# Kernel tuning notes

Hardware: AMD Instinct MI355X
Metric: run time of the kernel (lower is better)

Reference implementation:

```python
import jax, jax.numpy as jnp
import numpy as np

IN = 128      # input_size
HID = 64      # fast_net hidden width
NFW = IN * HID + HID  # 8256 flat fast weights (layer1 then layer2)
B = 256


def setup_inputs() -> dict:
    key = jax.random.key(0)
    k1, k2, k3, k4 = jax.random.split(key, 4)
    x = jax.random.normal(k1, (B, 1, IN), dtype=jnp.float32)
    # updater network weights: Linear(IN, 2*NFW, bias=False) then Linear(2*NFW, NFW, bias=False)
    W1 = jax.random.normal(k2, (2 * NFW, IN), dtype=jnp.float32) * 0.02
    W2 = jax.random.normal(k3, (NFW, 2 * NFW), dtype=jnp.float32) * 0.02
    # initial flat fast weights, in (0,1) since the update squashes there
    fw0 = jax.random.uniform(k4, (NFW,), dtype=jnp.float32)
    return {"x": x, "W1": W1, "W2": W2, "fw0": fw0}


def reference(x, W1, W2, fw0):
    xs = x[:, 0, :]  # [B, IN]
    # updater network has no weight updates itself -> batch the two matmuls
    U = (xs @ W1.T) @ W2.T  # [B, NFW] per-sample weight updates
    gain, shift = jnp.float32(10.0), jnp.float32(0.5)

    def step(fw, inp):
        x_i, u_i = inp
        # update_func: 1 / (1 + exp(-10*(w + u - 0.5)))
        fw = jax.nn.sigmoid(gain * (fw + u_i - shift))
        w1 = fw[: IN * HID].reshape(HID, IN)   # fast layer 1 [HID, IN]
        w2 = fw[IN * HID:].reshape(1, HID)     # fast layer 2 [1, HID]
        pred = w2 @ jax.nn.relu(w1 @ x_i)      # [1]
        return fw, pred

    _, preds = jax.lax.scan(step, fw0, (xs, U))  # sequential over batch, state persists
    return preds  # [B, 1]
```

## Files before the change

kernel.cpp:

```cpp
#include <hip/hip_runtime.h>
#include <hip/hip_bf16.h>

#define IN_DIM 128
#define HID    64
#define NFW    8256
#define BATCH  256
#define K2     16512
#define BM     96
#define NMB    86
#define KSPLIT 6
#define NT_PER 43
#define GRID_M 516

typedef float f32x4 __attribute__((ext_vector_type(4)));
typedef short bf16x8 __attribute__((ext_vector_type(8)));

__device__ __forceinline__ unsigned int f2bf(float f) {
    union { float f; unsigned int u; } v; v.f = f;
    return (v.u + 0x7FFFu + ((v.u >> 16) & 1u)) >> 16;
}

__global__ __launch_bounds__(256) void k_prep_w1t(const float* __restrict__ W1,
                                                  unsigned short* __restrict__ W1T) {
    __shared__ float tile[64][IN_DIM + 1];
    const int kt = blockIdx.x;
    const int t  = threadIdx.x;
    const float* src = W1 + (size_t)kt * 64 * IN_DIM;
#pragma unroll
    for (int p = 0; p < 8; ++p) {
        int c4 = p * 256 + t;
        int e = c4 * 4;
        int row = e >> 7, col = e & 127;
        f32x4 v = *reinterpret_cast<const f32x4*>(src + row * IN_DIM + col);
        tile[row][col+0] = v.x; tile[row][col+1] = v.y;
        tile[row][col+2] = v.z; tile[row][col+3] = v.w;
    }
    __syncthreads();
    unsigned short* dst = W1T + (size_t)kt * (IN_DIM * 64);
#pragma unroll
    for (int it = 0; it < 4; ++it) {
        int c = it * 256 + t;
        int n = c >> 3, kl0 = (c & 7) * 8;
        uint4 w;
        w.x = f2bf(tile[kl0+0][n]) | (f2bf(tile[kl0+1][n]) << 16);
        w.y = f2bf(tile[kl0+2][n]) | (f2bf(tile[kl0+3][n]) << 16);
        w.z = f2bf(tile[kl0+4][n]) | (f2bf(tile[kl0+5][n]) << 16);
        w.w = f2bf(tile[kl0+6][n]) | (f2bf(tile[kl0+7][n]) << 16);
        *reinterpret_cast<uint4*>(dst + c * 8) = w;
    }
}

__global__ __launch_bounds__(256, 2) void k_gemm_M(const float* __restrict__ W2,
                                                   const unsigned short* __restrict__ W1T,
                                                   float* __restrict__ Mpart) {
    __shared__ __align__(16) unsigned char smem[57344];
    float* trs = reinterpret_cast<float*>(smem);

    const int t = threadIdx.x;
    const int lane = t & 63, wid = t >> 6;
    const int wm = wid >> 1, wn = wid & 1;
    const int l15 = lane & 15, l4 = (lane >> 4) & 3;

    const int b = blockIdx.x;
    const int xcd = b & 7, slot = b >> 3;
    const int p = (xcd < 4) ? (xcd * 65 + slot) : (260 + (xcd - 4) * 64 + slot);
    const int ks = p / NMB, mb = p % NMB;

    const int m0 = mb * BM;
    const int g0 = ks * NT_PER;
    const int kt0 = (p * 7) % NT_PER;

    const int ar  = t >> 3;
    const int asw = (ar & 7) << 4;
    const float* abase = W2 + (size_t)(m0 + ar) * K2 + (size_t)g0 * 64 + (t & 7) * 8;
    const int bn  = t >> 1;
    const int bsw = (bn & 7) << 4;
    const unsigned short* bbase = W1T + (size_t)g0 * 8192 + bn * 64 + (t & 1) * 32;

    f32x4 sa0, sa1, sa2, sa3, sa4, sa5;
    uint4 sb0, sb1, sb2, sb3;
    f32x4 acc[3][4];
#pragma unroll
    for (int mf = 0; mf < 3; ++mf)
#pragma unroll
        for (int nf = 0; nf < 4; ++nf)
            acc[mf][nf] = (f32x4){0.f, 0.f, 0.f, 0.f};

#define LOADREGS(KT) {                                                         \
    const float* _ap = abase + (size_t)(KT) * 64;                              \
    sa0 = *reinterpret_cast<const f32x4*>(_ap);                                \
    sa1 = *reinterpret_cast<const f32x4*>(_ap + 4);                            \
    sa2 = *reinterpret_cast<const f32x4*>(_ap + (size_t)32 * K2);              \
    sa3 = *reinterpret_cast<const f32x4*>(_ap + (size_t)32 * K2 + 4);          \
    sa4 = *reinterpret_cast<const f32x4*>(_ap + (size_t)64 * K2);              \
    sa5 = *reinterpret_cast<const f32x4*>(_ap + (size_t)64 * K2 + 4);          \
    const unsigned short* _bp = bbase + (size_t)(KT) * 8192;                   \
    sb0 = *reinterpret_cast<const uint4*>(_bp);                                \
    sb1 = *reinterpret_cast<const uint4*>(_bp + 8);                            \
    sb2 = *reinterpret_cast<const uint4*>(_bp + 16);                           \
    sb3 = *reinterpret_cast<const uint4*>(_bp + 24); }

#define CVT16(W, LO, HI) { W.x = f2bf(LO.x) | (f2bf(LO.y) << 16);              \
                           W.y = f2bf(LO.z) | (f2bf(LO.w) << 16);              \
                           W.z = f2bf(HI.x) | (f2bf(HI.y) << 16);              \
                           W.w = f2bf(HI.z) | (f2bf(HI.w) << 16); }

#define STOREREGS(BUF) {                                                       \
    unsigned char* _Ash = smem + (BUF) * 12288;                                \
    unsigned char* _Bsh = smem + 24576 + (BUF) * 16384;                        \
    uint4 _w;                                                                  \
    const int _abyte = (t & 7) * 16;                                           \
    CVT16(_w, sa0, sa1);                                                       \
    *reinterpret_cast<uint4*>(&_Ash[(ar)      * 128 + (_abyte ^ asw)]) = _w;   \
    CVT16(_w, sa2, sa3);                                                       \
    *reinterpret_cast<uint4*>(&_Ash[(ar + 32) * 128 + (_abyte ^ asw)]) = _w;   \
    CVT16(_w, sa4, sa5);                                                       \
    *reinterpret_cast<uint4*>(&_Ash[(ar + 64) * 128 + (_abyte ^ asw)]) = _w;   \
    const int _bb = (t & 1) * 64;                                              \
    *reinterpret_cast<uint4*>(&_Bsh[bn * 128 + ((_bb)      ^ bsw)]) = sb0;     \
    *reinterpret_cast<uint4*>(&_Bsh[bn * 128 + ((_bb + 16) ^ bsw)]) = sb1;     \
    *reinterpret_cast<uint4*>(&_Bsh[bn * 128 + ((_bb + 32) ^ bsw)]) = sb2;     \
    *reinterpret_cast<uint4*>(&_Bsh[bn * 128 + ((_bb + 48) ^ bsw)]) = sb3; }

#define MFMA_PHASE(BUF) {                                                      \
    const unsigned char* _Ash = smem + (BUF) * 12288;                          \
    const unsigned char* _Bsh = smem + 24576 + (BUF) * 16384;                  \
    const int _fsw = (l15 & 7) << 4;                                           \
    _Pragma("unroll")                                                          \
    for (int kk = 0; kk < 2; ++kk) {                                           \
        const int _fc = (kk * 64 + l4 * 16) ^ _fsw;                            \
        bf16x8 af0 = *reinterpret_cast<const bf16x8*>(                         \
            &_Ash[(wm * 48 +  0 + l15) * 128 + _fc]);                          \
        bf16x8 af1 = *reinterpret_cast<const bf16x8*>(                         \
            &_Ash[(wm * 48 + 16 + l15) * 128 + _fc]);                          \
        bf16x8 af2 = *reinterpret_cast<const bf16x8*>(                         \
            &_Ash[(wm * 48 + 32 + l15) * 128 + _fc]);                          \
        bf16x8 bf0 = *reinterpret_cast<const bf16x8*>(                         \
            &_Bsh[(wn * 64 +  0 + l15) * 128 + _fc]);                          \
        bf16x8 bf1 = *reinterpret_cast<const bf16x8*>(                         \
            &_Bsh[(wn * 64 + 16 + l15) * 128 + _fc]);                          \
        bf16x8 bf2 = *reinterpret_cast<const bf16x8*>(                         \
            &_Bsh[(wn * 64 + 32 + l15) * 128 + _fc]);                          \
        bf16x8 bf3 = *reinterpret_cast<const bf16x8*>(                         \
            &_Bsh[(wn * 64 + 48 + l15) * 128 + _fc]);                          \
        acc[0][0] = __builtin_amdgcn_mfma_f32_16x16x32_bf16(af0, bf0, acc[0][0], 0, 0, 0); \
        acc[0][1] = __builtin_amdgcn_mfma_f32_16x16x32_bf16(af0, bf1, acc[0][1], 0, 0, 0); \
        acc[0][2] = __builtin_amdgcn_mfma_f32_16x16x32_bf16(af0, bf2, acc[0][2], 0, 0, 0); \
        acc[0][3] = __builtin_amdgcn_mfma_f32_16x16x32_bf16(af0, bf3, acc[0][3], 0, 0, 0); \
        acc[1][0] = __builtin_amdgcn_mfma_f32_16x16x32_bf16(af1, bf0, acc[1][0], 0, 0, 0); \
        acc[1][1] = __builtin_amdgcn_mfma_f32_16x16x32_bf16(af1, bf1, acc[1][1], 0, 0, 0); \
        acc[1][2] = __builtin_amdgcn_mfma_f32_16x16x32_bf16(af1, bf2, acc[1][2], 0, 0, 0); \
        acc[1][3] = __builtin_amdgcn_mfma_f32_16x16x32_bf16(af1, bf3, acc[1][3], 0, 0, 0); \
        acc[2][0] = __builtin_amdgcn_mfma_f32_16x16x32_bf16(af2, bf0, acc[2][0], 0, 0, 0); \
        acc[2][1] = __builtin_amdgcn_mfma_f32_16x16x32_bf16(af2, bf1, acc[2][1], 0, 0, 0); \
        acc[2][2] = __builtin_amdgcn_mfma_f32_16x16x32_bf16(af2, bf2, acc[2][2], 0, 0, 0); \
        acc[2][3] = __builtin_amdgcn_mfma_f32_16x16x32_bf16(af2, bf3, acc[2][3], 0, 0, 0); \
    } }

#define LBAR() { asm volatile("s_waitcnt lgkmcnt(0)" ::: "memory");            \
                 __builtin_amdgcn_s_barrier();                                 \
                 __builtin_amdgcn_sched_barrier(0); }

    int kreg = kt0;
    LOADREGS(kreg);
    STOREREGS(0);
    { int kn = kreg + 1; if (kn >= NT_PER) kn = 0; kreg = kn; }
    LOADREGS(kreg);
    LBAR();

    int cur = 0;
#pragma unroll 1
    for (int i = 0; i < NT_PER; ++i) {
        MFMA_PHASE(cur);
        __builtin_amdgcn_sched_barrier(0);
        if (i + 1 < NT_PER) {
            STOREREGS(cur ^ 1);
        }
        if (i + 2 < NT_PER) {
            int kn = kreg + 1; if (kn >= NT_PER) kn = 0; kreg = kn;
            LOADREGS(kreg);
        }
        LBAR();
        cur ^= 1;
    }

    float* outp = Mpart + (size_t)ks * ((size_t)NFW * IN_DIM) + (size_t)m0 * IN_DIM;
#pragma unroll 1
    for (int w = 0; w < 2; ++w) {
        __syncthreads();
        if (wm == w) {
#pragma unroll
            for (int mf = 0; mf < 3; ++mf)
#pragma unroll
                for (int nf = 0; nf < 4; ++nf)
#pragma unroll
                    for (int r = 0; r < 4; ++r)
                        trs[(mf * 16 + l4 * 4 + r) * 132 + wn * 64 + nf * 16 + l15] = acc[mf][nf][r];
        }
        __syncthreads();
#pragma unroll
        for (int q = 0; q < 6; ++q) {
            int idx = q * 256 + t;
            int rr = idx >> 5, c4 = (idx & 31) << 2;
            f32x4 v = *reinterpret_cast<const f32x4*>(&trs[rr * 132 + c4]);
            *reinterpret_cast<f32x4*>(outp + (size_t)(w * 48 + rr) * IN_DIM + c4) = v;
        }
    }
#undef LOADREGS
#undef CVT16
#undef STOREREGS
#undef MFMA_PHASE
#undef LBAR
}

__global__ __launch_bounds__(256) void k_reduce_M(const float* __restrict__ Mpart,
                                                  unsigned short* __restrict__ Mb) {
    const int idx = blockIdx.x * 256 + threadIdx.x;
    f32x4 s = (f32x4){0.f, 0.f, 0.f, 0.f};
#pragma unroll
    for (int ks = 0; ks < KSPLIT; ++ks) {
        f32x4 v = *reinterpret_cast<const f32x4*>(
            Mpart + (size_t)ks * ((size_t)NFW * IN_DIM) + (size_t)idx * 4);
        s.x += v.x; s.y += v.y; s.z += v.z; s.w += v.w;
    }
    uint2 o;
    o.x = f2bf(s.x) | (f2bf(s.y) << 16);
    o.y = f2bf(s.z) | (f2bf(s.w) << 16);
    *reinterpret_cast<uint2*>(Mb + (size_t)idx * 4) = o;
}

__global__ __launch_bounds__(256) void k_uchains(const float* __restrict__ xs,
                                                 const unsigned short* __restrict__ Mb,
                                                 const float* __restrict__ fw0,
                                                 float* __restrict__ FW) {
    __shared__ float Ulds[256][68];
    const int t = threadIdx.x, lane = t & 63, wid = t >> 6;
    const int l15 = lane & 15, l4 = (lane >> 4) & 3;
    const int j0 = blockIdx.x * 64;

    bf16x8 bfr[4][4];
#pragma unroll
    for (int kk = 0; kk < 4; ++kk)
#pragma unroll
        for (int nf = 0; nf < 4; ++nf)
            bfr[kk][nf] = *reinterpret_cast<const bf16x8*>(
                Mb + (size_t)(j0 + nf * 16 + l15) * IN_DIM + kk * 32 + l4 * 8);

#pragma unroll 1
    for (int ib = 0; ib < 4; ++ib) {
        const int i0 = wid * 64 + ib * 16;
        f32x4 acc[4];
#pragma unroll
        for (int nf = 0; nf < 4; ++nf) acc[nf] = (f32x4){0.f, 0.f, 0.f, 0.f};
#pragma unroll
        for (int kk = 0; kk < 4; ++kk) {
            const float* xp = xs + (size_t)(i0 + l15) * IN_DIM + kk * 32 + l4 * 8;
            f32x4 x0 = *reinterpret_cast<const f32x4*>(xp);
            f32x4 x1 = *reinterpret_cast<const f32x4*>(xp + 4);
            union { bf16x8 v; unsigned short s[8]; } af;
            af.s[0] = f2bf(x0.x); af.s[1] = f2bf(x0.y);
            af.s[2] = f2bf(x0.z); af.s[3] = f2bf(x0.w);
            af.s[4] = f2bf(x1.x); af.s[5] = f2bf(x1.y);
            af.s[6] = f2bf(x1.z); af.s[7] = f2bf(x1.w);
#pragma unroll
            for (int nf = 0; nf < 4; ++nf)
                acc[nf] = __builtin_amdgcn_mfma_f32_16x16x32_bf16(af.v, bfr[kk][nf], acc[nf], 0, 0, 0);
        }
#pragma unroll
        for (int nf = 0; nf < 4; ++nf)
#pragma unroll
            for (int r = 0; r < 4; ++r)
                Ulds[i0 + l4 * 4 + r][nf * 16 + l15] = acc[nf][r];
    }
    __syncthreads();

    if (wid == 0) {
        const int j = j0 + lane;
        float fw = fw0[j];
        float* fp = FW + j;
#pragma unroll 8
        for (int i = 0; i < BATCH; ++i) {
            float u = Ulds[i][lane];
            float z = 10.0f * (fw + u - 0.5f);
            fw = 1.0f / (1.0f + __expf(-z));
            fp[(size_t)i * NFW] = fw;
        }
    }
}

__global__ __launch_bounds__(256) void k_preds(const float* __restrict__ FW,
                                               const float* __restrict__ xs,
                                               float* __restrict__ out) {
    __shared__ float xsh[IN_DIM];
    __shared__ float hsh[HID];
    const int i = blockIdx.x, t = threadIdx.x;
    if (t < 32) {
        f32x4 v = *reinterpret_cast<const f32x4*>(xs + (size_t)i * IN_DIM + t * 4);
        xsh[t*4+0] = v.x; xsh[t*4+1] = v.y; xsh[t*4+2] = v.z; xsh[t*4+3] = v.w;
    }
    __syncthreads();
    const int k = t >> 2, q = t & 3;
    const float* fr = FW + (size_t)i * NFW + k * IN_DIM + q * 32;
    float p = 0.f;
#pragma unroll
    for (int m = 0; m < 8; ++m) {
        f32x4 v = *reinterpret_cast<const f32x4*>(fr + m * 4);
        const int d = q * 32 + m * 4;
        p += v.x * xsh[d] + v.y * xsh[d+1] + v.z * xsh[d+2] + v.w * xsh[d+3];
    }
    p += __shfl_xor(p, 1);
    p += __shfl_xor(p, 2);
    if (q == 0) hsh[k] = fmaxf(p, 0.f);
    __syncthreads();
    if (t < 64) {
        float v = FW[(size_t)i * NFW + IN_DIM * HID + t] * hsh[t];
        v += __shfl_xor(v, 1);  v += __shfl_xor(v, 2);  v += __shfl_xor(v, 4);
        v += __shfl_xor(v, 8);  v += __shfl_xor(v, 16); v += __shfl_xor(v, 32);
        if (t == 0) out[i] = v;
    }
}

extern "C" void kernel_launch(void* const* d_in, const int* in_sizes, int n_in,
                              void* d_out, int out_size, void* d_ws, size_t ws_size,
                              hipStream_t stream) {
    const float* x   = (const float*)d_in[0];
    const float* W1  = (const float*)d_in[1];
    const float* W2  = (const float*)d_in[2];
    const float* fw0 = (const float*)d_in[3];
    float* out = (float*)d_out;

    char* ws = (char*)d_ws;
    unsigned short* W1T   = (unsigned short*)(ws);
    float*          Mpart = (float*)(ws + 4227072);
    unsigned short* Mb    = (unsigned short*)(ws + 29589504);
    float*          FW    = (float*)(ws + 31703040);

    hipLaunchKernelGGL(k_prep_w1t, dim3(258),    dim3(256), 0, stream, W1, W1T);
    hipLaunchKernelGGL(k_gemm_M,   dim3(GRID_M), dim3(256), 0, stream, W2, W1T, Mpart);
    hipLaunchKernelGGL(k_reduce_M, dim3(1032),   dim3(256), 0, stream, Mpart, Mb);
    hipLaunchKernelGGL(k_uchains,  dim3(129),    dim3(256), 0, stream, x, Mb, fw0, FW);
    hipLaunchKernelGGL(k_preds,    dim3(256),    dim3(256), 0, stream, FW, x, out);
}
```

Baseline: 184.0 us.

## Retile W2·W1 GEMM to 64-row blocks with 4-way K split and 128-wide A loads

The M = W2·W1 GEMM now uses 64-row M tiles with a 4-way K split instead of 96-row tiles with a 6-way split. A is loaded as 128-column stripes per wave, 16 rows by 2 floats per lane, and stored to shared memory in two halves across two 64-wide phases. Shared memory per block shrinks and the occupancy hint rises to 3 blocks per CU. The smaller K split means fewer partial sums for the reduce kernel to read, and the longer row stripes are meant to make W2 reads more contiguous. In exchange the K ranges are uneven (33 vs 32 stripes) and the staging logic is more complex.

```diff
diff --git a/kernel.cpp b/kernel.cpp
--- a/kernel.cpp
+++ b/kernel.cpp
@@ -6,13 +6,13 @@
 #define NFW    8256
 #define BATCH  256
 #define K2     16512
-#define BM     96
-#define NMB    86
-#define KSPLIT 6
-#define NT_PER 43
+#define BM     64
+#define NMB    129
+#define KSPLIT 4
 #define GRID_M 516
 
 typedef float f32x4 __attribute__((ext_vector_type(4)));
+typedef float f32x2 __attribute__((ext_vector_type(2)));
 typedef short bf16x8 __attribute__((ext_vector_type(8)));
 
 __device__ __forceinline__ unsigned int f2bf(float f) {
@@ -50,10 +50,10 @@
     }
 }
 
-__global__ __launch_bounds__(256, 2) void k_gemm_M(const float* __restrict__ W2,
+__global__ __launch_bounds__(256, 3) void k_gemm_M(const float* __restrict__ W2,
                                                    const unsigned short* __restrict__ W1T,
                                                    float* __restrict__ Mpart) {
-    __shared__ __align__(16) unsigned char smem[57344];
+    __shared__ __align__(16) unsigned char smem[49152];
     float* trs = reinterpret_cast<float*>(smem);
 
     const int t = threadIdx.x;
@@ -67,55 +67,68 @@
     const int ks = p / NMB, mb = p % NMB;
 
     const int m0 = mb * BM;
-    const int g0 = ks * NT_PER;
-    const int kt0 = (p * 7) % NT_PER;
-
-    const int ar  = t >> 3;
-    const int asw = (ar & 7) << 4;
-    const float* abase = W2 + (size_t)(m0 + ar) * K2 + (size_t)g0 * 64 + (t & 7) * 8;
+    const int NS = (ks == 0) ? 33 : 32;
+    const int g0 = (ks == 0) ? 0 : (32 * ks + 1);
+    const int st0 = (p * 7) % NS;
+
+    const float* abase = W2 + (size_t)(m0 + wid * 16) * K2 + lane * 2;
     const int bn  = t >> 1;
     const int bsw = (bn & 7) << 4;
-    const unsigned short* bbase = W1T + (size_t)g0 * 8192 + bn * 64 + (t & 1) * 32;
-
-    f32x4 sa0, sa1, sa2, sa3, sa4, sa5;
+    const unsigned short* bbase = W1T + bn * 64 + (t & 1) * 32;
+
+    f32x2 ra0, ra1, ra2, ra3, ra4, ra5, ra6, ra7;
+    f32x2 ra8, ra9, ra10, ra11, ra12, ra13, ra14, ra15;
     uint4 sb0, sb1, sb2, sb3;
-    f32x4 acc[3][4];
-#pragma unroll
-    for (int mf = 0; mf < 3; ++mf)
+    f32x4 acc[2][4];
+#pragma unroll
+    for (int mf = 0; mf < 2; ++mf)
 #pragma unroll
         for (int nf = 0; nf < 4; ++nf)
             acc[mf][nf] = (f32x4){0.f, 0.f, 0.f, 0.f};
 
-#define LOADREGS(KT) {                                                         \
-    const float* _ap = abase + (size_t)(KT) * 64;                              \
-    sa0 = *reinterpret_cast<const f32x4*>(_ap);                                \
-    sa1 = *reinterpret_cast<const f32x4*>(_ap + 4);                            \
-    sa2 = *reinterpret_cast<const f32x4*>(_ap + (size_t)32 * K2);              \
-    sa3 = *reinterpret_cast<const f32x4*>(_ap + (size_t)32 * K2 + 4);          \
-    sa4 = *reinterpret_cast<const f32x4*>(_ap + (size_t)64 * K2);              \
-    sa5 = *reinterpret_cast<const f32x4*>(_ap + (size_t)64 * K2 + 4);          \
+#define LOADA(S) {                                                             \
+    const float* _ap = abase + (size_t)(S) * 128;                              \
+    ra0  = *reinterpret_cast<const f32x2*>(_ap);                               \
+    ra1  = *reinterpret_cast<const f32x2*>(_ap + (size_t)1  * K2);             \
+    ra2  = *reinterpret_cast<const f32x2*>(_ap + (size_t)2  * K2);             \
+    ra3  = *reinterpret_cast<const f32x2*>(_ap + (size_t)3  * K2);             \
+    ra4  = *reinterpret_cast<const f32x2*>(_ap + (size_t)4  * K2);             \
+    ra5  = *reinterpret_cast<const f32x2*>(_ap + (size_t)5  * K2);             \
+    ra6  = *reinterpret_cast<const f32x2*>(_ap + (size_t)6  * K2);             \
+    ra7  = *reinterpret_cast<const f32x2*>(_ap + (size_t)7  * K2);             \
+    ra8  = *reinterpret_cast<const f32x2*>(_ap + (size_t)8  * K2);             \
+    ra9  = *reinterpret_cast<const f32x2*>(_ap + (size_t)9  * K2);             \
+    ra10 = *reinterpret_cast<const f32x2*>(_ap + (size_t)10 * K2);             \
+    ra11 = *reinterpret_cast<const f32x2*>(_ap + (size_t)11 * K2);             \
+    ra12 = *reinterpret_cast<const f32x2*>(_ap + (size_t)12 * K2);             \
+    ra13 = *reinterpret_cast<const f32x2*>(_ap + (size_t)13 * K2);             \
+    ra14 = *reinterpret_cast<const f32x2*>(_ap + (size_t)14 * K2);             \
+    ra15 = *reinterpret_cast<const f32x2*>(_ap + (size_t)15 * K2); }
+
+#define LOADB(KT) {                                                            \
     const unsigned short* _bp = bbase + (size_t)(KT) * 8192;                   \
     sb0 = *reinterpret_cast<const uint4*>(_bp);                                \
     sb1 = *reinterpret_cast<const uint4*>(_bp + 8);                            \
     sb2 = *reinterpret_cast<const uint4*>(_bp + 16);                           \
     sb3 = *reinterpret_cast<const uint4*>(_bp + 24); }
 
-#define CVT16(W, LO, HI) { W.x = f2bf(LO.x) | (f2bf(LO.y) << 16);              \
-                           W.y = f2bf(LO.z) | (f2bf(LO.w) << 16);              \
-                           W.z = f2bf(HI.x) | (f2bf(HI.y) << 16);              \
-                           W.w = f2bf(HI.z) | (f2bf(HI.w) << 16); }
-
-#define STOREREGS(BUF) {                                                       \
-    unsigned char* _Ash = smem + (BUF) * 12288;                                \
-    unsigned char* _Bsh = smem + 24576 + (BUF) * 16384;                        \
-    uint4 _w;                                                                  \
-    const int _abyte = (t & 7) * 16;                                           \
-    CVT16(_w, sa0, sa1);                                                       \
-    *reinterpret_cast<uint4*>(&_Ash[(ar)      * 128 + (_abyte ^ asw)]) = _w;   \
-    CVT16(_w, sa2, sa3);                                                       \
-    *reinterpret_cast<uint4*>(&_Ash[(ar + 32) * 128 + (_abyte ^ asw)]) = _w;   \
-    CVT16(_w, sa4, sa5);                                                       \
-    *reinterpret_cast<uint4*>(&_Ash[(ar + 64) * 128 + (_abyte ^ asw)]) = _w;   \
+#define STA1(BUF, L, RA) {                                                     \
+    unsigned int _v = f2bf(RA.x) | (f2bf(RA.y) << 16);                         \
+    *reinterpret_cast<unsigned int*>(&smem[(BUF) * 8192 +                      \
+        (wid * 16 + (L)) * 128 + (((lane & 31) * 4) ^ (((L) & 7) << 4))]) = _v; }
+
+#define STOREA_HALF(BUF, H) {                                                  \
+    if ((lane >> 5) == (H)) {                                                  \
+        STA1(BUF, 0,  ra0)  STA1(BUF, 1,  ra1)  STA1(BUF, 2,  ra2)             \
+        STA1(BUF, 3,  ra3)  STA1(BUF, 4,  ra4)  STA1(BUF, 5,  ra5)             \
+        STA1(BUF, 6,  ra6)  STA1(BUF, 7,  ra7)  STA1(BUF, 8,  ra8)             \
+        STA1(BUF, 9,  ra9)  STA1(BUF, 10, ra10) STA1(BUF, 11, ra11)            \
+        STA1(BUF, 12, ra12) STA1(BUF, 13, ra13) STA1(BUF, 14, ra14)            \
+        STA1(BUF, 15, ra15)                                                    \
+    } }
+
+#define STOREB(BUF) {                                                          \
+    unsigned char* _Bsh = smem + 16384 + (BUF) * 16384;                        \
     const int _bb = (t & 1) * 64;                                              \
     *reinterpret_cast<uint4*>(&_Bsh[bn * 128 + ((_bb)      ^ bsw)]) = sb0;     \
     *reinterpret_cast<uint4*>(&_Bsh[bn * 128 + ((_bb + 16) ^ bsw)]) = sb1;     \
@@ -123,18 +136,16 @@
     *reinterpret_cast<uint4*>(&_Bsh[bn * 128 + ((_bb + 48) ^ bsw)]) = sb3; }
 
 #define MFMA_PHASE(BUF) {                                                      \
-    const unsigned char* _Ash = smem + (BUF) * 12288;                          \
-    const unsigned char* _Bsh = smem + 24576 + (BUF) * 16384;                  \
+    const unsigned char* _Ash = smem + (BUF) * 8192;                           \
+    const unsigned char* _Bsh = smem + 16384 + (BUF) * 16384;                  \
     const int _fsw = (l15 & 7) << 4;                                           \
     _Pragma("unroll")                                                          \
     for (int kk = 0; kk < 2; ++kk) {                                           \
         const int _fc = (kk * 64 + l4 * 16) ^ _fsw;                            \
         bf16x8 af0 = *reinterpret_cast<const bf16x8*>(                         \
-            &_Ash[(wm * 48 +  0 + l15) * 128 + _fc]);                          \
+            &_Ash[(wm * 32 +  0 + l15) * 128 + _fc]);                          \
         bf16x8 af1 = *reinterpret_cast<const bf16x8*>(                         \
-            &_Ash[(wm * 48 + 16 + l15) * 128 + _fc]);                          \
-        bf16x8 af2 = *reinterpret_cast<const bf16x8*>(                         \
-            &_Ash[(wm * 48 + 32 + l15) * 128 + _fc]);                          \
+            &_Ash[(wm * 32 + 16 + l15) * 128 + _fc]);                          \
         bf16x8 bf0 = *reinterpret_cast<const bf16x8*>(                         \
             &_Bsh[(wn * 64 +  0 + l15) * 128 + _fc]);                          \
         bf16x8 bf1 = *reinterpret_cast<const bf16x8*>(                         \
@@ -151,34 +162,46 @@
         acc[1][1] = __builtin_amdgcn_mfma_f32_16x16x32_bf16(af1, bf1, acc[1][1], 0, 0, 0); \
         acc[1][2] = __builtin_amdgcn_mfma_f32_16x16x32_bf16(af1, bf2, acc[1][2], 0, 0, 0); \
         acc[1][3] = __builtin_amdgcn_mfma_f32_16x16x32_bf16(af1, bf3, acc[1][3], 0, 0, 0); \
-        acc[2][0] = __builtin_amdgcn_mfma_f32_16x16x32_bf16(af2, bf0, acc[2][0], 0, 0, 0); \
-        acc[2][1] = __builtin_amdgcn_mfma_f32_16x16x32_bf16(af2, bf1, acc[2][1], 0, 0, 0); \
-        acc[2][2] = __builtin_amdgcn_mfma_f32_16x16x32_bf16(af2, bf2, acc[2][2], 0, 0, 0); \
-        acc[2][3] = __builtin_amdgcn_mfma_f32_16x16x32_bf16(af2, bf3, acc[2][3], 0, 0, 0); \
     } }
 
 #define LBAR() { asm volatile("s_waitcnt lgkmcnt(0)" ::: "memory");            \
                  __builtin_amdgcn_s_barrier();                                 \
                  __builtin_amdgcn_sched_barrier(0); }
 
-    int kreg = kt0;
-    LOADREGS(kreg);
-    STOREREGS(0);
-    { int kn = kreg + 1; if (kn >= NT_PER) kn = 0; kreg = kn; }
-    LOADREGS(kreg);
+    {
+        const int S0 = g0 + st0;
+        LOADA(S0);
+        LOADB(2 * S0);
+        STOREA_HALF(0, 0);
+        STOREB(0);
+        LOADB(2 * S0 + 1);
+    }
     LBAR();
+    int sNrel = st0 + 1; if (sNrel >= NS) sNrel = 0;
 
     int cur = 0;
 #pragma unroll 1
-    for (int i = 0; i < NT_PER; ++i) {
+    for (int ph = 0; ph < 2 * NS; ++ph) {
         MFMA_PHASE(cur);
         __builtin_amdgcn_sched_barrier(0);
-        if (i + 1 < NT_PER) {
-            STOREREGS(cur ^ 1);
-        }
-        if (i + 2 < NT_PER) {
-            int kn = kreg + 1; if (kn >= NT_PER) kn = 0; kreg = kn;
-            LOADREGS(kreg);
+        if (ph + 1 < 2 * NS) {
+            if ((ph & 1) == 0) {
+                STOREA_HALF(cur ^ 1, 1);
+                STOREB(cur ^ 1);
+                if (ph + 2 < 2 * NS) {
+                    const int Sn = g0 + sNrel;
+                    LOADA(Sn);
+                    LOADB(2 * Sn);
+                }
+            } else {
+                STOREA_HALF(cur ^ 1, 0);
+                STOREB(cur ^ 1);
+                if (ph + 2 < 2 * NS) {
+                    const int Sn = g0 + sNrel;
+                    LOADB(2 * Sn + 1);
+                    sNrel = sNrel + 1; if (sNrel >= NS) sNrel = 0;
+                }
+            }
         }
         LBAR();
         cur ^= 1;
@@ -190,7 +213,7 @@
         __syncthreads();
         if (wm == w) {
 #pragma unroll
-            for (int mf = 0; mf < 3; ++mf)
+            for (int mf = 0; mf < 2; ++mf)
 #pragma unroll
                 for (int nf = 0; nf < 4; ++nf)
 #pragma unroll
@@ -199,16 +222,18 @@
         }
         __syncthreads();
 #pragma unroll
-        for (int q = 0; q < 6; ++q) {
+        for (int q = 0; q < 4; ++q) {
             int idx = q * 256 + t;
             int rr = idx >> 5, c4 = (idx & 31) << 2;
             f32x4 v = *reinterpret_cast<const f32x4*>(&trs[rr * 132 + c4]);
-            *reinterpret_cast<f32x4*>(outp + (size_t)(w * 48 + rr) * IN_DIM + c4) = v;
-        }
-    }
-#undef LOADREGS
-#undef CVT16
-#undef STOREREGS
+            *reinterpret_cast<f32x4*>(outp + (size_t)(w * 32 + rr) * IN_DIM + c4) = v;
+        }
+    }
+#undef LOADA
+#undef LOADB
+#undef STA1
+#undef STOREA_HALF
+#undef STOREB
 #undef MFMA_PHASE
 #undef LBAR
 }
@@ -332,8 +357,8 @@
     char* ws = (char*)d_ws;
     unsigned short* W1T   = (unsigned short*)(ws);
     float*          Mpart = (float*)(ws + 4227072);
-    unsigned short* Mb    = (unsigned short*)(ws + 29589504);
-    float*          FW    = (float*)(ws + 31703040);
+    unsigned short* Mb    = (unsigned short*)(ws + 21135360);
+    float*          FW    = (float*)(ws + 23248896);
 
     hipLaunchKernelGGL(k_prep_w1t, dim3(258),    dim3(256), 0, stream, W1, W1T);
     hipLaunchKernelGGL(k_gemm_M,   dim3(GRID_M), dim3(256), 0, stream, W2, W1T, Mpart);
```

Result: slower. 211.1 us (+14.8%).

## Stream GEMM tiles to LDS via global_load_lds and shrink M tile

Applied to the files above, without the earlier changes.

The W2×W1T GEMM now copies fp32 W2 and bf16 W1T tiles straight into swizzled shared memory with global_load_lds, instead of staging them through registers. The fp32-to-bf16 conversion of A moves into the MFMA phase, done after reading from LDS. The M tile shrinks from 96 to 64 rows, which raises the grid to 774 blocks with a new XCD mapping. The aim is fewer staging registers and VALU conversion work on the load path, plus more blocks in flight. In exchange, A takes twice the LDS space and bandwidth (fp32), the kernel drops the occupancy-2 launch bound and uses 64KB of LDS, and the synchronisation is simpler with no explicit vmcnt wait before the barrier.

```diff
diff --git a/kernel.cpp b/kernel.cpp
--- a/kernel.cpp
+++ b/kernel.cpp
@@ -6,11 +6,11 @@
 #define NFW    8256
 #define BATCH  256
 #define K2     16512
-#define BM     96
-#define NMB    86
+#define BM     64
+#define NMB    129
 #define KSPLIT 6
 #define NT_PER 43
-#define GRID_M 516
+#define GRID_M 774
 
 typedef float f32x4 __attribute__((ext_vector_type(4)));
 typedef short bf16x8 __attribute__((ext_vector_type(8)));
@@ -19,6 +19,20 @@
     union { float f; unsigned int u; } v; v.f = f;
     return (v.u + 0x7FFFu + ((v.u >> 16) & 1u)) >> 16;
 }
+
+__device__ __forceinline__ bf16x8 pack8(f32x4 a, f32x4 b) {
+    union { bf16x8 v; __hip_bfloat162 h[4]; } u;
+    u.h[0] = __float22bfloat162_rn(float2{a.x, a.y});
+    u.h[1] = __float22bfloat162_rn(float2{a.z, a.w});
+    u.h[2] = __float22bfloat162_rn(float2{b.x, b.y});
+    u.h[3] = __float22bfloat162_rn(float2{b.z, b.w});
+    return u.v;
+}
+
+#define GLL16(SRC, DST)                                                        \
+    __builtin_amdgcn_global_load_lds(                                          \
+        (const __attribute__((address_space(1))) unsigned int*)(SRC),          \
+        (__attribute__((address_space(3))) unsigned int*)(DST), 16, 0, 0)
 
 __global__ __launch_bounds__(256) void k_prep_w1t(const float* __restrict__ W1,
                                                   unsigned short* __restrict__ W1T) {
@@ -50,10 +64,10 @@
     }
 }
 
-__global__ __launch_bounds__(256, 2) void k_gemm_M(const float* __restrict__ W2,
-                                                   const unsigned short* __restrict__ W1T,
-                                                   float* __restrict__ Mpart) {
-    __shared__ __align__(16) unsigned char smem[57344];
+__global__ __launch_bounds__(256) void k_gemm_M(const float* __restrict__ W2,
+                                                const unsigned short* __restrict__ W1T,
+                                                float* __restrict__ Mpart) {
+    __shared__ __align__(16) unsigned char smem[65536];
     float* trs = reinterpret_cast<float*>(smem);
 
     const int t = threadIdx.x;
@@ -63,86 +77,78 @@
 
     const int b = blockIdx.x;
     const int xcd = b & 7, slot = b >> 3;
-    const int p = (xcd < 4) ? (xcd * 65 + slot) : (260 + (xcd - 4) * 64 + slot);
+    const int p = (xcd < 6) ? (xcd * 97 + slot) : (582 + (xcd - 6) * 96 + slot);
     const int ks = p / NMB, mb = p % NMB;
 
     const int m0 = mb * BM;
     const int g0 = ks * NT_PER;
     const int kt0 = (p * 7) % NT_PER;
 
-    const int ar  = t >> 3;
-    const int asw = (ar & 7) << 4;
-    const float* abase = W2 + (size_t)(m0 + ar) * K2 + (size_t)g0 * 64 + (t & 7) * 8;
-    const int bn  = t >> 1;
-    const int bsw = (bn & 7) << 4;
-    const unsigned short* bbase = W1T + (size_t)g0 * 8192 + bn * 64 + (t & 1) * 32;
-
-    f32x4 sa0, sa1, sa2, sa3, sa4, sa5;
-    uint4 sb0, sb1, sb2, sb3;
-    f32x4 acc[3][4];
-#pragma unroll
-    for (int mf = 0; mf < 3; ++mf)
+    const int ca0 = wid * 4;
+    const int rl0 = 4 * (ca0 + 0) + (lane >> 4);
+    const int rl1 = 4 * (ca0 + 1) + (lane >> 4);
+    const int rl2 = 4 * (ca0 + 2) + (lane >> 4);
+    const int rl3 = 4 * (ca0 + 3) + (lane >> 4);
+    const int acb = (lane & 15) * 16;
+    const float* aS0 = W2 + (size_t)(m0 + rl0) * K2 + (size_t)g0 * 64 + ((acb ^ ((rl0 & 7) << 4)) >> 2);
+    const float* aS1 = W2 + (size_t)(m0 + rl1) * K2 + (size_t)g0 * 64 + ((acb ^ ((rl1 & 7) << 4)) >> 2);
+    const float* aS2 = W2 + (size_t)(m0 + rl2) * K2 + (size_t)g0 * 64 + ((acb ^ ((rl2 & 7) << 4)) >> 2);
+    const float* aS3 = W2 + (size_t)(m0 + rl3) * K2 + (size_t)g0 * 64 + ((acb ^ ((rl3 & 7) << 4)) >> 2);
+    const int rb0 = 8 * (ca0 + 0) + (lane >> 3);
+    const int rb1 = 8 * (ca0 + 1) + (lane >> 3);
+    const int rb2 = 8 * (ca0 + 2) + (lane >> 3);
+    const int rb3 = 8 * (ca0 + 3) + (lane >> 3);
+    const int bcb = (lane & 7) * 16;
+    const unsigned short* bS0 = W1T + (size_t)g0 * 8192 + rb0 * 64 + ((bcb ^ ((rb0 & 7) << 4)) >> 1);
+    const unsigned short* bS1 = W1T + (size_t)g0 * 8192 + rb1 * 64 + ((bcb ^ ((rb1 & 7) << 4)) >> 1);
+    const unsigned short* bS2 = W1T + (size_t)g0 * 8192 + rb2 * 64 + ((bcb ^ ((rb2 & 7) << 4)) >> 1);
+    const unsigned short* bS3 = W1T + (size_t)g0 * 8192 + rb3 * 64 + ((bcb ^ ((rb3 & 7) << 4)) >> 1);
+    const int aD = ca0 * 1024;
+
+    f32x4 acc[2][4];
+#pragma unroll
+    for (int mf = 0; mf < 2; ++mf)
 #pragma unroll
         for (int nf = 0; nf < 4; ++nf)
             acc[mf][nf] = (f32x4){0.f, 0.f, 0.f, 0.f};
 
-#define LOADREGS(KT) {                                                         \
-    const float* _ap = abase + (size_t)(KT) * 64;                              \
-    sa0 = *reinterpret_cast<const f32x4*>(_ap);                                \
-    sa1 = *reinterpret_cast<const f32x4*>(_ap + 4);                            \
-    sa2 = *reinterpret_cast<const f32x4*>(_ap + (size_t)32 * K2);              \
-    sa3 = *reinterpret_cast<const f32x4*>(_ap + (size_t)32 * K2 + 4);          \
-    sa4 = *reinterpret_cast<const f32x4*>(_ap + (size_t)64 * K2);              \
-    sa5 = *reinterpret_cast<const f32x4*>(_ap + (size_t)64 * K2 + 4);          \
-    const unsigned short* _bp = bbase + (size_t)(KT) * 8192;                   \
-    sb0 = *reinterpret_cast<const uint4*>(_bp);                                \
-    sb1 = *reinterpret_cast<const uint4*>(_bp + 8);                            \
-    sb2 = *reinterpret_cast<const uint4*>(_bp + 16);                           \
-    sb3 = *reinterpret_cast<const uint4*>(_bp + 24); }
-
-#define CVT16(W, LO, HI) { W.x = f2bf(LO.x) | (f2bf(LO.y) << 16);              \
-                           W.y = f2bf(LO.z) | (f2bf(LO.w) << 16);              \
-                           W.z = f2bf(HI.x) | (f2bf(HI.y) << 16);              \
-                           W.w = f2bf(HI.z) | (f2bf(HI.w) << 16); }
-
-#define STOREREGS(BUF) {                                                       \
-    unsigned char* _Ash = smem + (BUF) * 12288;                                \
-    unsigned char* _Bsh = smem + 24576 + (BUF) * 16384;                        \
-    uint4 _w;                                                                  \
-    const int _abyte = (t & 7) * 16;                                           \
-    CVT16(_w, sa0, sa1);                                                       \
-    *reinterpret_cast<uint4*>(&_Ash[(ar)      * 128 + (_abyte ^ asw)]) = _w;   \
-    CVT16(_w, sa2, sa3);                                                       \
-    *reinterpret_cast<uint4*>(&_Ash[(ar + 32) * 128 + (_abyte ^ asw)]) = _w;   \
-    CVT16(_w, sa4, sa5);                                                       \
-    *reinterpret_cast<uint4*>(&_Ash[(ar + 64) * 128 + (_abyte ^ asw)]) = _w;   \
-    const int _bb = (t & 1) * 64;                                              \
-    *reinterpret_cast<uint4*>(&_Bsh[bn * 128 + ((_bb)      ^ bsw)]) = sb0;     \
-    *reinterpret_cast<uint4*>(&_Bsh[bn * 128 + ((_bb + 16) ^ bsw)]) = sb1;     \
-    *reinterpret_cast<uint4*>(&_Bsh[bn * 128 + ((_bb + 32) ^ bsw)]) = sb2;     \
-    *reinterpret_cast<uint4*>(&_Bsh[bn * 128 + ((_bb + 48) ^ bsw)]) = sb3; }
+#define ISSUE_AB(BUF, KT) {                                                    \
+    unsigned char* _ab = smem + (BUF) * 16384;                                 \
+    unsigned char* _bb = smem + 32768 + (BUF) * 16384;                         \
+    const size_t _ao = (size_t)(KT) * 64;                                      \
+    const size_t _bo = (size_t)(KT) * 8192;                                    \
+    GLL16(aS0 + _ao, _ab + aD);                                                \
+    GLL16(aS1 + _ao, _ab + aD + 1024);                                         \
+    GLL16(aS2 + _ao, _ab + aD + 2048);                                         \
+    GLL16(aS3 + _ao, _ab + aD + 3072);                                         \
+    GLL16(bS0 + _bo, _bb + aD);                                                \
+    GLL16(bS1 + _bo, _bb + aD + 1024);                                         \
+    GLL16(bS2 + _bo, _bb + aD + 2048);                                         \
+    GLL16(bS3 + _bo, _bb + aD + 3072);                                         \
+}
 
 #define MFMA_PHASE(BUF) {                                                      \
-    const unsigned char* _Ash = smem + (BUF) * 12288;                          \
-    const unsigned char* _Bsh = smem + 24576 + (BUF) * 16384;                  \
-    const int _fsw = (l15 & 7) << 4;                                           \
+    const unsigned char* _Ash = smem + (BUF) * 16384;                          \
+    const unsigned char* _Bsh = smem + 32768 + (BUF) * 16384;                  \
     _Pragma("unroll")                                                          \
     for (int kk = 0; kk < 2; ++kk) {                                           \
-        const int _fc = (kk * 64 + l4 * 16) ^ _fsw;                            \
-        bf16x8 af0 = *reinterpret_cast<const bf16x8*>(                         \
-            &_Ash[(wm * 48 +  0 + l15) * 128 + _fc]);                          \
-        bf16x8 af1 = *reinterpret_cast<const bf16x8*>(                         \
-            &_Ash[(wm * 48 + 16 + l15) * 128 + _fc]);                          \
-        bf16x8 af2 = *reinterpret_cast<const bf16x8*>(                         \
-            &_Ash[(wm * 48 + 32 + l15) * 128 + _fc]);                          \
-        bf16x8 bf0 = *reinterpret_cast<const bf16x8*>(                         \
-            &_Bsh[(wn * 64 +  0 + l15) * 128 + _fc]);                          \
-        bf16x8 bf1 = *reinterpret_cast<const bf16x8*>(                         \
-            &_Bsh[(wn * 64 + 16 + l15) * 128 + _fc]);                          \
-        bf16x8 bf2 = *reinterpret_cast<const bf16x8*>(                         \
-            &_Bsh[(wn * 64 + 32 + l15) * 128 + _fc]);                          \
-        bf16x8 bf3 = *reinterpret_cast<const bf16x8*>(                         \
-            &_Bsh[(wn * 64 + 48 + l15) * 128 + _fc]);                          \
+        const int _ar0 = wm * 32 + l15;                                        \
+        const int _ar1 = wm * 32 + 16 + l15;                                   \
+        const int _pb  = kk * 128 + l4 * 32;                                   \
+        const int _s0  = (_ar0 & 7) << 4;                                      \
+        const int _s1  = (_ar1 & 7) << 4;                                      \
+        f32x4 _x0 = *reinterpret_cast<const f32x4*>(&_Ash[_ar0 * 256 + ((_pb)      ^ _s0)]); \
+        f32x4 _x1 = *reinterpret_cast<const f32x4*>(&_Ash[_ar0 * 256 + ((_pb + 16) ^ _s0)]); \
+        f32x4 _y0 = *reinterpret_cast<const f32x4*>(&_Ash[_ar1 * 256 + ((_pb)      ^ _s1)]); \
+        f32x4 _y1 = *reinterpret_cast<const f32x4*>(&_Ash[_ar1 * 256 + ((_pb + 16) ^ _s1)]); \
+        bf16x8 af0 = pack8(_x0, _x1);                                          \
+        bf16x8 af1 = pack8(_y0, _y1);                                          \
+        const int _fsw = (l15 & 7) << 4;                                       \
+        const int _fc  = (kk * 64 + l4 * 16) ^ _fsw;                           \
+        bf16x8 bf0 = *reinterpret_cast<const bf16x8*>(&_Bsh[(wn * 64 +  0 + l15) * 128 + _fc]); \
+        bf16x8 bf1 = *reinterpret_cast<const bf16x8*>(&_Bsh[(wn * 64 + 16 + l15) * 128 + _fc]); \
+        bf16x8 bf2 = *reinterpret_cast<const bf16x8*>(&_Bsh[(wn * 64 + 32 + l15) * 128 + _fc]); \
+        bf16x8 bf3 = *reinterpret_cast<const bf16x8*>(&_Bsh[(wn * 64 + 48 + l15) * 128 + _fc]); \
         acc[0][0] = __builtin_amdgcn_mfma_f32_16x16x32_bf16(af0, bf0, acc[0][0], 0, 0, 0); \
         acc[0][1] = __builtin_amdgcn_mfma_f32_16x16x32_bf16(af0, bf1, acc[0][1], 0, 0, 0); \
         acc[0][2] = __builtin_amdgcn_mfma_f32_16x16x32_bf16(af0, bf2, acc[0][2], 0, 0, 0); \
@@ -151,36 +157,22 @@
         acc[1][1] = __builtin_amdgcn_mfma_f32_16x16x32_bf16(af1, bf1, acc[1][1], 0, 0, 0); \
         acc[1][2] = __builtin_amdgcn_mfma_f32_16x16x32_bf16(af1, bf2, acc[1][2], 0, 0, 0); \
         acc[1][3] = __builtin_amdgcn_mfma_f32_16x16x32_bf16(af1, bf3, acc[1][3], 0, 0, 0); \
-        acc[2][0] = __builtin_amdgcn_mfma_f32_16x16x32_bf16(af2, bf0, acc[2][0], 0, 0, 0); \
-        acc[2][1] = __builtin_amdgcn_mfma_f32_16x16x32_bf16(af2, bf1, acc[2][1], 0, 0, 0); \
-        acc[2][2] = __builtin_amdgcn_mfma_f32_16x16x32_bf16(af2, bf2, acc[2][2], 0, 0, 0); \
-        acc[2][3] = __builtin_amdgcn_mfma_f32_16x16x32_bf16(af2, bf3, acc[2][3], 0, 0, 0); \
     } }
 
-#define LBAR() { asm volatile("s_waitcnt lgkmcnt(0)" ::: "memory");            \
-                 __builtin_amdgcn_s_barrier();                                 \
-                 __builtin_amdgcn_sched_barrier(0); }
-
-    int kreg = kt0;
-    LOADREGS(kreg);
-    STOREREGS(0);
-    { int kn = kreg + 1; if (kn >= NT_PER) kn = 0; kreg = kn; }
-    LOADREGS(kreg);
-    LBAR();
+    int tcur = kt0;
+    ISSUE_AB(0, tcur);
+    __syncthreads();
 
     int cur = 0;
 #pragma unroll 1
     for (int i = 0; i < NT_PER; ++i) {
+        if (i + 1 < NT_PER) {
+            int tn = tcur + 1; if (tn >= NT_PER) tn = 0;
+            ISSUE_AB(cur ^ 1, tn);
+            tcur = tn;
+        }
         MFMA_PHASE(cur);
-        __builtin_amdgcn_sched_barrier(0);
-        if (i + 1 < NT_PER) {
-            STOREREGS(cur ^ 1);
-        }
-        if (i + 2 < NT_PER) {
-            int kn = kreg + 1; if (kn >= NT_PER) kn = 0; kreg = kn;
-            LOADREGS(kreg);
-        }
-        LBAR();
+        __syncthreads();
         cur ^= 1;
     }
 
@@ -190,7 +182,7 @@
         __syncthreads();
         if (wm == w) {
 #pragma unroll
-            for (int mf = 0; mf < 3; ++mf)
+            for (int mf = 0; mf < 2; ++mf)
 #pragma unroll
                 for (int nf = 0; nf < 4; ++nf)
 #pragma unroll
@@ -199,18 +191,15 @@
         }
         __syncthreads();
 #pragma unroll
-        for (int q = 0; q < 6; ++q) {
+        for (int q = 0; q < 4; ++q) {
             int idx = q * 256 + t;
             int rr = idx >> 5, c4 = (idx & 31) << 2;
             f32x4 v = *reinterpret_cast<const f32x4*>(&trs[rr * 132 + c4]);
-            *reinterpret_cast<f32x4*>(outp + (size_t)(w * 48 + rr) * IN_DIM + c4) = v;
-        }
-    }
-#undef LOADREGS
-#undef CVT16
-#undef STOREREGS
+            *reinterpret_cast<f32x4*>(outp + (size_t)(w * 32 + rr) * IN_DIM + c4) = v;
+        }
+    }
+#undef ISSUE_AB
 #undef MFMA_PHASE
-#undef LBAR
 }
 
 __global__ __launch_bounds__(256) void k_reduce_M(const float* __restrict__ Mpart,
```

New measurement: 165.5 us. 1.11x faster.
